# Performance work log

Hardware: AMD Instinct MI355X
Metric: run time of the kernel (lower is better)

Reference implementation:

```python
import jax, jax.numpy as jnp
import numpy as np

N, F, H, K_SUB, DEPTH = 500_000, 64, 32, 16, 4
N_NODES = 2 ** DEPTH - 1   # 15 internal nodes
N_LEAVES = 2 ** DEPTH      # 16 leaves
SLOPE = 0.01               # torch LeakyReLU default negative_slope


def _leaky(v):
    return jnp.where(v >= 0, v, SLOPE * v)


def setup_inputs() -> dict:
    key = jax.random.key(0)
    ks = jax.random.split(key, 8)
    x = jax.random.normal(ks[0], (N, F), dtype=jnp.float32)
    subset_idx = jax.random.randint(ks[1], (N_NODES, K_SUB), 0, F, dtype=jnp.int32)
    W1 = jax.random.normal(ks[2], (N_NODES, H, K_SUB), dtype=jnp.float32) * (1.0 / np.sqrt(K_SUB))
    b1 = jnp.zeros((N_NODES, H), jnp.float32)
    W2 = jax.random.normal(ks[3], (N_NODES, H, H), dtype=jnp.float32) * (1.0 / np.sqrt(H))
    b2 = jnp.zeros((N_NODES, H), jnp.float32)
    W3 = jax.random.normal(ks[4], (N_NODES, 2, H), dtype=jnp.float32) * (1.0 / np.sqrt(H))
    b3 = jnp.zeros((N_NODES, 2), jnp.float32)
    # leaf 'best' constants (class modes precomputed by populate_best)
    leaf_best = jax.random.randint(ks[5], (N_LEAVES,), 0, 10).astype(jnp.float32)
    return {"x": x, "W1": W1, "b1": b1, "W2": W2, "b2": b2, "W3": W3, "b3": b3,
            "leaf_best": leaf_best, "subset_idx": subset_idx}


def _forward(x, W1, b1, W2, b2, W3, b3, leaf_best, subset_idx):
    n = x.shape[0]
    loc = jnp.zeros((n,), jnp.int32)   # local node index within current level
    off = 0
    for level in range(DEPTH):
        k = 2 ** level
        sl = slice(off, off + k)
        xs = x[:, subset_idx[sl]]                                   # [N, k, K_SUB]
        h = _leaky(jnp.einsum('nkf,khf->nkh', xs, W1[sl]) + b1[sl])  # [N, k, H]
        h = _leaky(jnp.einsum('nkh,kgh->nkg', h, W2[sl]) + b2[sl])   # [N, k, H]
        logits = jnp.einsum('nkh,koh->nko', h, W3[sl]) + b3[sl]      # [N, k, 2]
        p0 = jax.nn.softmax(logits, axis=-1)[..., 0]                 # [N, k]
        p0_row = jnp.take_along_axis(p0, loc[:, None], axis=1)[:, 0]
        bit = (p0_row < 0.5).astype(jnp.int32)  # 0 -> left, 1 -> right
        loc = 2 * loc + bit
        off += k
    return leaf_best[loc]  # [N]


def reference(x, W1, b1, W2, b2, W3, b3, leaf_best, subset_idx):
    return _forward(x, W1, b1, W2, b2, W3, b3, leaf_best, subset_idx)
```

## Files before the change

kernel.cpp:

```cpp
#include <hip/hip_runtime.h>

#define NF 64
#define NH 32
#define NK 16
#define NNODES 15
#define BLOCK 512
#define NWAVES (BLOCK / 64)


__global__ __attribute__((amdgpu_flat_work_group_size(512, 512),
                          amdgpu_waves_per_eu(2, 4)))
void tree_mlp_kernel(
    const float* __restrict__ x,
    const float* __restrict__ W1, const float* __restrict__ b1,
    const float* __restrict__ W2, const float* __restrict__ b2,
    const float* __restrict__ W3, const float* __restrict__ b3,
    const float* __restrict__ leaf_best, const int* __restrict__ subset_idx,
    float* __restrict__ out, int N)
{
    __shared__ __align__(16) float W2L[NNODES * 1024];
    __shared__ int      subL[NNODES * NK];
    __shared__ unsigned permL[BLOCK];
    __shared__ int      sortL[NWAVES * 16];

    const int tid  = threadIdx.x;
    const int lane = tid & 63;
    const int wv   = tid >> 6;

    for (int i = tid; i < NNODES * 1024; i += BLOCK) W2L[i] = W2[i];
    for (int i = tid; i < NNODES * NK;   i += BLOCK) subL[i] = subset_idx[i];
    __syncthreads();

    const int s = blockIdx.x * BLOCK + tid;
    int valid = (s < N) ? 1 : 0;
    int id    = valid ? s : 0;
    int loc = 0, off = 0;

    #pragma unroll 1
    for (int level = 0; level < 4; ++level) {
        if (level > 0) {
            const int nb = 1 << level;
            int myrank = 0;
            #pragma unroll 1
            for (int b = 0; b < nb; ++b) {
                const unsigned long long m = __ballot(loc == b);
                if (loc == b)
                    myrank = __popcll(m & ((1ull << lane) - 1ull));
                if (lane == 0)
                    sortL[b * NWAVES + wv] = __popcll(m);
            }
            __syncthreads();
            if (tid == 0) {
                int run = 0;
                for (int i = 0; i < nb * NWAVES; ++i) {
                    const int c = sortL[i];
                    sortL[i] = run;
                    run += c;
                }
            }
            __syncthreads();
            const int slot = sortL[loc * NWAVES + wv] + myrank;
            permL[slot] = ((unsigned)id << 5) | ((unsigned)valid << 4) | (unsigned)loc;
            __syncthreads();
            const unsigned p = permL[tid];
            id    = (int)(p >> 5);
            valid = (int)((p >> 4) & 1u);
            loc   = (int)(p & 15u);
            __syncthreads();
        }

        const int node = off + loc;
        const float* xr = x + (size_t)id * NF;

        float xs[NK];
        const int* si = subL + node * NK;
        #pragma unroll
        for (int k = 0; k < NK; ++k) xs[k] = xr[si[k]];

        float h1v[NH];
        const float4* w1g = (const float4*)(W1 + node * (NH * NK));
        const float* b1g = b1 + node * NH;
        #pragma unroll
        for (int j = 0; j < NH; ++j) {
            float acc = b1g[j];
            #pragma unroll
            for (int q = 0; q < NK / 4; ++q) {
                const float4 t = w1g[j * 4 + q];
                acc += t.x * xs[q * 4 + 0];
                acc += t.y * xs[q * 4 + 1];
                acc += t.z * xs[q * 4 + 2];
                acc += t.w * xs[q * 4 + 3];
            }
            h1v[j] = (acc >= 0.f) ? acc : 0.01f * acc;
        }

        float h2v[NH];
        const float4* w2n = (const float4*)(W2L + node * 1024);
        const float* b2g = b2 + node * NH;
        #pragma unroll
        for (int g = 0; g < NH; ++g) {
            float acc = b2g[g];
            #pragma unroll
            for (int q = 0; q < NH / 4; ++q) {
                const float4 t = w2n[g * 8 + q];
                acc += t.x * h1v[q * 4 + 0];
                acc += t.y * h1v[q * 4 + 1];
                acc += t.z * h1v[q * 4 + 2];
                acc += t.w * h1v[q * 4 + 3];
            }
            h2v[g] = (acc >= 0.f) ? acc : 0.01f * acc;
        }

        const float4* w3g = (const float4*)(W3 + node * 2 * NH);
        float l0 = b3[node * 2 + 0];
        float l1 = b3[node * 2 + 1];
        #pragma unroll
        for (int q = 0; q < NH / 4; ++q) {
            const float4 t0 = w3g[q];
            l0 += t0.x * h2v[q * 4 + 0];
            l0 += t0.y * h2v[q * 4 + 1];
            l0 += t0.z * h2v[q * 4 + 2];
            l0 += t0.w * h2v[q * 4 + 3];
        }
        #pragma unroll
        for (int q = 0; q < NH / 4; ++q) {
            const float4 t1 = w3g[8 + q];
            l1 += t1.x * h2v[q * 4 + 0];
            l1 += t1.y * h2v[q * 4 + 1];
            l1 += t1.z * h2v[q * 4 + 2];
            l1 += t1.w * h2v[q * 4 + 3];
        }

        const int bit = (l0 < l1) ? 1 : 0;
        loc = 2 * loc + bit;
        off = 2 * off + 1;
    }

    if (valid) out[id] = leaf_best[loc];
}

extern "C" void kernel_launch(void* const* d_in, const int* in_sizes, int n_in,
                              void* d_out, int out_size, void* d_ws, size_t ws_size,
                              hipStream_t stream) {
    const float* x         = (const float*)d_in[0];
    const float* W1        = (const float*)d_in[1];
    const float* b1        = (const float*)d_in[2];
    const float* W2        = (const float*)d_in[3];
    const float* b2        = (const float*)d_in[4];
    const float* W3        = (const float*)d_in[5];
    const float* b3        = (const float*)d_in[6];
    const float* leaf_best = (const float*)d_in[7];
    const int*   subset    = (const int*)d_in[8];

    const int N = in_sizes[0] / NF;
    const int grid = (N + BLOCK - 1) / BLOCK;
    tree_mlp_kernel<<<grid, BLOCK, 0, stream>>>(
        x, W1, b1, W2, b2, W3, b3, leaf_best, subset, (float*)d_out, N);
}
```

Baseline: 499.0 us.

## Read wave-uniform node weights as scalar loads instead of staging W2 in LDS

Drops the per-block copy of all W2 matrices into LDS. Each wave now loops over the distinct nodes its lanes hold, using readfirstlane so that W1, W2, W3, biases and subset indices become wave-uniform scalar loads. The serial single-thread prefix sum becomes a wave shuffle scan, one barrier is removed, and waves_per_eu is raised because LDS use is much smaller. Waves whose lanes span several nodes repeat the whole MLP once per node, which adds redundant compute.

```diff
diff --git a/kernel.cpp b/kernel.cpp
--- a/kernel.cpp
+++ b/kernel.cpp
@@ -3,13 +3,12 @@
 #define NF 64
 #define NH 32
 #define NK 16
-#define NNODES 15
 #define BLOCK 512
 #define NWAVES (BLOCK / 64)
 
 
-__global__ __attribute__((amdgpu_flat_work_group_size(512, 512),
-                          amdgpu_waves_per_eu(2, 4)))
+__global__ __attribute__((amdgpu_flat_work_group_size(BLOCK, BLOCK),
+                          amdgpu_waves_per_eu(4, 8)))
 void tree_mlp_kernel(
     const float* __restrict__ x,
     const float* __restrict__ W1, const float* __restrict__ b1,
@@ -18,18 +17,12 @@
     const float* __restrict__ leaf_best, const int* __restrict__ subset_idx,
     float* __restrict__ out, int N)
 {
-    __shared__ __align__(16) float W2L[NNODES * 1024];
-    __shared__ int      subL[NNODES * NK];
     __shared__ unsigned permL[BLOCK];
-    __shared__ int      sortL[NWAVES * 16];
+    __shared__ int      sortL[64];
 
     const int tid  = threadIdx.x;
     const int lane = tid & 63;
     const int wv   = tid >> 6;
-
-    for (int i = tid; i < NNODES * 1024; i += BLOCK) W2L[i] = W2[i];
-    for (int i = tid; i < NNODES * NK;   i += BLOCK) subL[i] = subset_idx[i];
-    __syncthreads();
 
     const int s = blockIdx.x * BLOCK + tid;
     int valid = (s < N) ? 1 : 0;
@@ -47,16 +40,19 @@
                 if (loc == b)
                     myrank = __popcll(m & ((1ull << lane) - 1ull));
                 if (lane == 0)
-                    sortL[b * NWAVES + wv] = __popcll(m);
+                    sortL[b * NWAVES + wv] = (int)__popcll(m);
             }
             __syncthreads();
-            if (tid == 0) {
-                int run = 0;
-                for (int i = 0; i < nb * NWAVES; ++i) {
-                    const int c = sortL[i];
-                    sortL[i] = run;
-                    run += c;
+            if (wv == 0) {
+                const int mcnt = nb * NWAVES;
+                const int cnt = (lane < mcnt) ? sortL[lane] : 0;
+                int v = cnt;
+                #pragma unroll
+                for (int d = 1; d < 64; d <<= 1) {
+                    const int t = __shfl_up(v, d);
+                    if (lane >= d) v += t;
                 }
+                if (lane < mcnt) sortL[lane] = v - cnt;
             }
             __syncthreads();
             const int slot = sortL[loc * NWAVES + wv] + myrank;
@@ -66,72 +62,59 @@
             id    = (int)(p >> 5);
             valid = (int)((p >> 4) & 1u);
             loc   = (int)(p & 15u);
-            __syncthreads();
         }
 
         const int node = off + loc;
-        const float* xr = x + (size_t)id * NF;
+        int bit = 0;
 
-        float xs[NK];
-        const int* si = subL + node * NK;
-        #pragma unroll
-        for (int k = 0; k < NK; ++k) xs[k] = xr[si[k]];
+        unsigned long long rem = ~0ull;
+        #pragma unroll 1
+        while (rem) {
+            const int lead = (int)__ffsll((long long)rem) - 1;
+            const int n0 = __builtin_amdgcn_readfirstlane(__shfl(node, lead));
+            const bool mine = (node == n0);
 
-        float h1v[NH];
-        const float4* w1g = (const float4*)(W1 + node * (NH * NK));
-        const float* b1g = b1 + node * NH;
-        #pragma unroll
-        for (int j = 0; j < NH; ++j) {
-            float acc = b1g[j];
+            const int* __restrict__ si = subset_idx + n0 * NK;
+            const float* __restrict__ xr = x + (size_t)id * NF;
+            float xs[NK];
             #pragma unroll
-            for (int q = 0; q < NK / 4; ++q) {
-                const float4 t = w1g[j * 4 + q];
-                acc += t.x * xs[q * 4 + 0];
-                acc += t.y * xs[q * 4 + 1];
-                acc += t.z * xs[q * 4 + 2];
-                acc += t.w * xs[q * 4 + 3];
+            for (int k = 0; k < NK; ++k) xs[k] = xr[si[k]];
+
+            const float* __restrict__ w1 = W1 + n0 * (NH * NK);
+            const float* __restrict__ bb1 = b1 + n0 * NH;
+            float h1v[NH];
+            #pragma unroll
+            for (int j = 0; j < NH; ++j) {
+                float acc = bb1[j];
+                #pragma unroll
+                for (int k = 0; k < NK; ++k) acc += w1[j * NK + k] * xs[k];
+                h1v[j] = fmaxf(acc, 0.01f * acc);
             }
-            h1v[j] = (acc >= 0.f) ? acc : 0.01f * acc;
+
+            const float* __restrict__ w2 = W2 + n0 * (NH * NH);
+            const float* __restrict__ bb2 = b2 + n0 * NH;
+            float h2v[NH];
+            #pragma unroll
+            for (int g = 0; g < NH; ++g) {
+                float acc = bb2[g];
+                #pragma unroll
+                for (int h = 0; h < NH; ++h) acc += w2[g * NH + h] * h1v[h];
+                h2v[g] = fmaxf(acc, 0.01f * acc);
+            }
+
+            const float* __restrict__ w3 = W3 + n0 * (2 * NH);
+            float l0 = b3[n0 * 2 + 0];
+            float l1 = b3[n0 * 2 + 1];
+            #pragma unroll
+            for (int h = 0; h < NH; ++h) {
+                l0 += w3[h]      * h2v[h];
+                l1 += w3[NH + h] * h2v[h];
+            }
+
+            if (mine) bit = (l0 < l1) ? 1 : 0;
+            rem &= ~__ballot(mine);
         }
 
-        float h2v[NH];
-        const float4* w2n = (const float4*)(W2L + node * 1024);
-        const float* b2g = b2 + node * NH;
-        #pragma unroll
-        for (int g = 0; g < NH; ++g) {
-            float acc = b2g[g];
-            #pragma unroll
-            for (int q = 0; q < NH / 4; ++q) {
-                const float4 t = w2n[g * 8 + q];
-                acc += t.x * h1v[q * 4 + 0];
-                acc += t.y * h1v[q * 4 + 1];
-                acc += t.z * h1v[q * 4 + 2];
-                acc += t.w * h1v[q * 4 + 3];
-            }
-            h2v[g] = (acc >= 0.f) ? acc : 0.01f * acc;
-        }
-
-        const float4* w3g = (const float4*)(W3 + node * 2 * NH);
-        float l0 = b3[node * 2 + 0];
-        float l1 = b3[node * 2 + 1];
-        #pragma unroll
-        for (int q = 0; q < NH / 4; ++q) {
-            const float4 t0 = w3g[q];
-            l0 += t0.x * h2v[q * 4 + 0];
-            l0 += t0.y * h2v[q * 4 + 1];
-            l0 += t0.z * h2v[q * 4 + 2];
-            l0 += t0.w * h2v[q * 4 + 3];
-        }
-        #pragma unroll
-        for (int q = 0; q < NH / 4; ++q) {
-            const float4 t1 = w3g[8 + q];
-            l1 += t1.x * h2v[q * 4 + 0];
-            l1 += t1.y * h2v[q * 4 + 1];
-            l1 += t1.z * h2v[q * 4 + 2];
-            l1 += t1.w * h2v[q * 4 + 3];
-        }
-
-        const int bit = (l0 < l1) ? 1 : 0;
         loc = 2 * loc + bit;
         off = 2 * off + 1;
     }
```

After: 838.3 us. +68.0%, slower.

## Drop LDS weight staging, read W2 from global, parallelize bucket prefix scan

Applied to the files above, without the earlier changes.

Removes the per-block copy of all W2 matrices and subset indices into shared memory, which used about 60KB of LDS. W2 and the indices are now read straight from global memory, where the lanes of a sorted wave mostly share one node and get cache hits. The serial single-thread prefix sum becomes a wave-level shuffle scan, one trailing barrier is dropped, and the occupancy hint rises to 4-8 waves per EU. The trade is more global and cache traffic for the weight reads, in exchange for higher occupancy and no startup copy per block.

```diff
diff --git a/kernel.cpp b/kernel.cpp
--- a/kernel.cpp
+++ b/kernel.cpp
@@ -3,13 +3,12 @@
 #define NF 64
 #define NH 32
 #define NK 16
-#define NNODES 15
 #define BLOCK 512
 #define NWAVES (BLOCK / 64)
 
 
-__global__ __attribute__((amdgpu_flat_work_group_size(512, 512),
-                          amdgpu_waves_per_eu(2, 4)))
+__global__ __attribute__((amdgpu_flat_work_group_size(BLOCK, BLOCK),
+                          amdgpu_waves_per_eu(4, 8)))
 void tree_mlp_kernel(
     const float* __restrict__ x,
     const float* __restrict__ W1, const float* __restrict__ b1,
@@ -18,18 +17,12 @@
     const float* __restrict__ leaf_best, const int* __restrict__ subset_idx,
     float* __restrict__ out, int N)
 {
-    __shared__ __align__(16) float W2L[NNODES * 1024];
-    __shared__ int      subL[NNODES * NK];
     __shared__ unsigned permL[BLOCK];
-    __shared__ int      sortL[NWAVES * 16];
+    __shared__ int      sortL[64];
 
     const int tid  = threadIdx.x;
     const int lane = tid & 63;
     const int wv   = tid >> 6;
-
-    for (int i = tid; i < NNODES * 1024; i += BLOCK) W2L[i] = W2[i];
-    for (int i = tid; i < NNODES * NK;   i += BLOCK) subL[i] = subset_idx[i];
-    __syncthreads();
 
     const int s = blockIdx.x * BLOCK + tid;
     int valid = (s < N) ? 1 : 0;
@@ -47,16 +40,19 @@
                 if (loc == b)
                     myrank = __popcll(m & ((1ull << lane) - 1ull));
                 if (lane == 0)
-                    sortL[b * NWAVES + wv] = __popcll(m);
+                    sortL[b * NWAVES + wv] = (int)__popcll(m);
             }
             __syncthreads();
-            if (tid == 0) {
-                int run = 0;
-                for (int i = 0; i < nb * NWAVES; ++i) {
-                    const int c = sortL[i];
-                    sortL[i] = run;
-                    run += c;
+            if (wv == 0) {
+                const int mcnt = nb * NWAVES;
+                const int cnt = (lane < mcnt) ? sortL[lane] : 0;
+                int v = cnt;
+                #pragma unroll
+                for (int d = 1; d < 64; d <<= 1) {
+                    const int t = __shfl_up(v, d);
+                    if (lane >= d) v += t;
                 }
+                if (lane < mcnt) sortL[lane] = v - cnt;
             }
             __syncthreads();
             const int slot = sortL[loc * NWAVES + wv] + myrank;
@@ -66,14 +62,13 @@
             id    = (int)(p >> 5);
             valid = (int)((p >> 4) & 1u);
             loc   = (int)(p & 15u);
-            __syncthreads();
         }
 
         const int node = off + loc;
         const float* xr = x + (size_t)id * NF;
 
         float xs[NK];
-        const int* si = subL + node * NK;
+        const int* si = subset_idx + node * NK;
         #pragma unroll
         for (int k = 0; k < NK; ++k) xs[k] = xr[si[k]];
 
@@ -95,14 +90,14 @@
         }
 
         float h2v[NH];
-        const float4* w2n = (const float4*)(W2L + node * 1024);
+        const float4* w2g = (const float4*)(W2 + node * (NH * NH));
         const float* b2g = b2 + node * NH;
         #pragma unroll
         for (int g = 0; g < NH; ++g) {
             float acc = b2g[g];
             #pragma unroll
             for (int q = 0; q < NH / 4; ++q) {
-                const float4 t = w2n[g * 8 + q];
+                const float4 t = w2g[g * 8 + q];
                 acc += t.x * h1v[q * 4 + 0];
                 acc += t.y * h1v[q * 4 + 1];
                 acc += t.z * h1v[q * 4 + 2];
```

Result: slower. 1.491 ms (+198.7%).
